# Kernel optimization log

Hardware: AMD Instinct MI355X
Metric: run time of the kernel (lower is better)

The kernel has to match this reference:

```python
import jax, jax.numpy as jnp
import numpy as np
from jax import lax

B, T, M = 32, 512, 512
D, DM, H, A = 256, 256, 256, 256  # input, memory, hidden, attention sizes
NEG = -1e30


def setup_inputs() -> dict:
    key = jax.random.key(0)
    ks = jax.random.split(key, 12)
    s = lambda k, shape, scale: jax.random.normal(k, shape, dtype=jnp.float32) * scale
    inp = {
        "inputs": s(ks[0], (B, T, D), 1.0),
        "inputs_mask": jnp.ones((B, T), dtype=bool),
        "memory": s(ks[1], (B, M, DM), 1.0),
        "memory_mask": jnp.ones((B, M), dtype=bool),
        # per-direction attention params (dir 0 = fw, 1 = bw)
        "Wm": s(ks[2], (2, DM, A), DM ** -0.5),
        "Wi": s(ks[3], (2, D, A), D ** -0.5),
        "Wh": s(ks[4], (2, H, A), H ** -0.5),
        "v": s(ks[5], (2, A), A ** -0.5),
        # per-direction GRUCell params, torch layout [3H, in] / [3H, H]
        "W_ih": s(ks[6], (2, 3 * H, D + DM), (D + DM) ** -0.5),
        "W_hh": s(ks[7], (2, 3 * H, H), H ** -0.5),
        "b_ih": s(ks[8], (2, 3 * H), 0.01),
        "b_hh": s(ks[9], (2, 3 * H), 0.01),
        # output gate: sigmoid(x @ Wg) * x on [B,T,2H]
        "Wg": s(ks[10], (2 * H, 2 * H), (2 * H) ** -0.5),
    }
    return inp


def _run_direction(xs, memory, memory_mask, Wm, Wi, Wh, v, W_ih, W_hh, b_ih, b_hh):
    # xs: [T,B,D] time-major. memory: [B,M,DM]. Returns [T,B,H].
    mem_proj = jnp.einsum("bmd,da->bma", memory, Wm)  # [B,M,A], hoisted out of loop

    def step(h, x_t):
        q = x_t @ Wi + h @ Wh                              # [B,A]
        s = jnp.einsum("bma,a->bm", jnp.tanh(mem_proj + q[:, None, :]), v)
        s = jnp.where(memory_mask, s, NEG)
        a = jax.nn.softmax(s, axis=-1)                     # [B,M]
        c = jnp.einsum("bm,bmd->bd", a, memory)            # [B,DM]
        xc = jnp.concatenate([x_t, c], axis=-1)            # [B,D+DM]
        gi = xc @ W_ih.T + b_ih
        gh = h @ W_hh.T + b_hh
        ir, iz, inn = jnp.split(gi, 3, axis=-1)
        hr, hz, hn = jnp.split(gh, 3, axis=-1)
        r = jax.nn.sigmoid(ir + hr)
        z = jax.nn.sigmoid(iz + hz)
        n = jnp.tanh(inn + r * hn)
        h_new = (1.0 - z) * n + z * h
        return h_new, h_new

    h0 = jnp.zeros((xs.shape[1], H), dtype=xs.dtype)
    _, ys = lax.scan(step, h0, xs)
    return ys


def reference(inputs, inputs_mask, memory, memory_mask, Wm, Wi, Wh, v,
              W_ih, W_hh, b_ih, b_hh, Wg):
    xs = jnp.transpose(inputs, (1, 0, 2))  # [T,B,D]
    y_fw = _run_direction(xs, memory, memory_mask, Wm[0], Wi[0], Wh[0], v[0],
                          W_ih[0], W_hh[0], b_ih[0], b_hh[0])
    y_bw = _run_direction(xs[::-1], memory, memory_mask, Wm[1], Wi[1], Wh[1], v[1],
                          W_ih[1], W_hh[1], b_ih[1], b_hh[1])[::-1]
    out = jnp.concatenate([y_fw, y_bw], axis=-1)       # [T,B,2H]
    out = jnp.transpose(out, (1, 0, 2))                # [B,T,2H]
    # Gate (dropout=0): sigmoid(W out) * out
    return jax.nn.sigmoid(out @ Wg) * out
```

## Files before the change

### kernel.cpp

```cpp
#include <hip/hip_runtime.h>
#include <stdint.h>

typedef unsigned short u16;
typedef unsigned int   u32;
typedef _Float16 half2v __attribute__((ext_vector_type(2)));

#define L2E 1.4426950408889634f
#define TWO_L2E 2.8853900817779268f

__device__ __forceinline__ float bf2f(u16 b){ return __uint_as_float(((u32)b) << 16); }
__device__ __forceinline__ float ldf(const void* p, size_t i, int flag){
  return flag ? ((const float*)p)[i] : bf2f(((const u16*)p)[i]);
}
__device__ __forceinline__ float rcpfast(float x){
#if __has_builtin(__builtin_amdgcn_rcpf)
  return __builtin_amdgcn_rcpf(x);
#else
  return 1.0f / x;
#endif
}
__device__ __forceinline__ float exp2fast(float x){
#if __has_builtin(__builtin_amdgcn_exp2f)
  return __builtin_amdgcn_exp2f(x);
#else
  return exp2f(x);
#endif
}
__device__ __forceinline__ float fdot2f(u32 a, u32 b, float c){
#if __has_builtin(__builtin_amdgcn_fdot2)
  return __builtin_amdgcn_fdot2(__builtin_bit_cast(half2v, a), __builtin_bit_cast(half2v, b), c, false);
#else
  half2v ha = __builtin_bit_cast(half2v, a), hb = __builtin_bit_cast(half2v, b);
  return c + (float)ha[0]*(float)hb[0] + (float)ha[1]*(float)hb[1];
#endif
}
__device__ __forceinline__ u32 pkh2(float lo, float hi){
  half2v h; h[0] = (_Float16)lo; h[1] = (_Float16)hi;
  return __builtin_bit_cast(u32, h);
}
__device__ __forceinline__ u16 f2h16(float f){
  _Float16 h = (_Float16)f;
  return __builtin_bit_cast(u16, h);
}
__device__ __forceinline__ float h16f(u16 h){
  return (float)__builtin_bit_cast(_Float16, h);
}

__global__ void k_sentinelf(float* __restrict__ out, int n, float val){
  int i = blockIdx.x*256 + threadIdx.x;
  if(i < n) out[i] = val;
}

__global__ void k_detect(const u16* __restrict__ p, int n, int* __restrict__ flag){
  __shared__ int cnt;
  if(threadIdx.x == 0) cnt = 0;
  __syncthreads();
  int c = 0;
  for(int i = threadIdx.x; i < n; i += 256){
    int e = (p[i] >> 7) & 0xFF;
    c += (e >= 112 && e <= 142) ? 1 : 0;
  }
  atomicAdd(&cnt, c);
  __syncthreads();
  if(threadIdx.x == 0) *flag = (cnt >= (n/10)*9) ? 0 : 1;
}
__global__ void k_convf(const void* __restrict__ src, float* __restrict__ dst, int n,
                        const int* __restrict__ flag){
  int i = blockIdx.x*256 + threadIdx.x;
  if(i < n) dst[i] = ldf(src, i, *flag);
}

__global__ void k_pack_wh2(const void* __restrict__ Wh, u32* __restrict__ out,
                           const int* __restrict__ flag){
  int i = blockIdx.x*256 + threadIdx.x;
  if(i >= 2*128*256) return;
  int d = i >> 15, k2 = (i >> 8) & 127, a = i & 255;
  float lo = ldf(Wh, ((size_t)d*256 + 2*k2    )*256 + a, *flag);
  float hi = ldf(Wh, ((size_t)d*256 + 2*k2 + 1)*256 + a, *flag);
  out[i] = pkh2(lo, hi);
}
__global__ void k_pack_wc2(const void* __restrict__ Whh, const void* __restrict__ Wih,
                           u32* __restrict__ out, const int* __restrict__ flag){
  int i = blockIdx.x*256 + threadIdx.x;
  if(i >= 2*128*2304) return;
  int d = i / (128*2304), r = i % (128*2304);
  int k2 = r / 2304, j = r % 2304;
  int k = 2*k2;
  float lo, hi;
  if(j < 768){
    lo = ldf(Whh, ((size_t)d*768 + j)*256 + k,     *flag);
    hi = ldf(Whh, ((size_t)d*768 + j)*256 + k + 1, *flag);
  } else if(j < 1536){
    lo = ldf(Wih, ((size_t)d*768 + (j-768))*512 + 256 + k,     *flag);
    hi = ldf(Wih, ((size_t)d*768 + (j-768))*512 + 256 + k + 1, *flag);
  } else {
    lo = ldf(Wih, ((size_t)d*768 + (j-1536))*512 + k,     *flag);
    hi = ldf(Wih, ((size_t)d*768 + (j-1536))*512 + k + 1, *flag);
  }
  out[i] = pkh2(lo, hi);
}
__global__ void k_pack_h2(const void* __restrict__ src, u32* __restrict__ out, int n2,
                          const int* __restrict__ flag){
  int i = blockIdx.x*256 + threadIdx.x;
  if(i >= n2) return;
  out[i] = pkh2(ldf(src, 2*(size_t)i, *flag), ldf(src, 2*(size_t)i + 1, *flag));
}
__global__ void k_pack_wiht(const void* __restrict__ Wih, float* __restrict__ out,
                            const int* __restrict__ flag){
  int i = blockIdx.x*256 + threadIdx.x;
  if(i >= 2*256*768) return;
  int d = i / 196608, r = i % 196608;
  int k = r / 768, j = r % 768;
  out[i] = ldf(Wih, ((size_t)d*768 + j)*512 + k, *flag);
}

template<int MODE>
__global__ __launch_bounds__(256)
void k_gemm_h16(const float* __restrict__ A, int lda,
                const float* __restrict__ B, int ldb,
                u16* __restrict__ C, int N, int K)
{
  __shared__ float As[64][17];
  __shared__ float Bs[16][65];
  const int m0 = blockIdx.x * 64, n0 = blockIdx.y * 64;
  const int tid = threadIdx.x;
  const int arow = tid >> 2, acol = (tid & 3) * 4;
  const int brow = tid >> 4, bcol = (tid & 15) * 4;
  const int ty = tid >> 4, tx = tid & 15;
  float acc[4][4];
  #pragma unroll
  for(int i=0;i<4;++i)
    #pragma unroll
    for(int j=0;j<4;++j) acc[i][j] = 0.f;
  for(int k0 = 0; k0 < K; k0 += 16){
    float4 a4 = *(const float4*)(A + (size_t)(m0 + arow)*lda + k0 + acol);
    As[arow][acol+0] = a4.x; As[arow][acol+1] = a4.y;
    As[arow][acol+2] = a4.z; As[arow][acol+3] = a4.w;
    float4 b4 = *(const float4*)(B + (size_t)(k0 + brow)*ldb + n0 + bcol);
    Bs[brow][bcol+0] = b4.x; Bs[brow][bcol+1] = b4.y;
    Bs[brow][bcol+2] = b4.z; Bs[brow][bcol+3] = b4.w;
    __syncthreads();
    #pragma unroll
    for(int kk = 0; kk < 16; ++kk){
      float ar[4], br[4];
      #pragma unroll
      for(int i=0;i<4;++i) ar[i] = As[ty*4+i][kk];
      #pragma unroll
      for(int j=0;j<4;++j) br[j] = Bs[kk][tx*4+j];
      #pragma unroll
      for(int i=0;i<4;++i)
        #pragma unroll
        for(int j=0;j<4;++j) acc[i][j] = fmaf(ar[i], br[j], acc[i][j]);
    }
    __syncthreads();
  }
  #pragma unroll
  for(int i=0;i<4;++i)
    #pragma unroll
    for(int j=0;j<4;++j){
      float v = acc[i][j];
      if(MODE==1){ v = exp2fast(v * TWO_L2E); v = fminf(v, 65504.f); }
      C[(size_t)(m0 + ty*4 + i)*N + n0 + tx*4 + j] = f2h16(v);
    }
}

template<int USE_GIX>
__global__ __launch_bounds__(1024)
void k_scan5(const u16* __restrict__ E16,
             const u16* __restrict__ qx16,
             const u32* __restrict__ Wh2,
             const u32* __restrict__ Wc2,
             const u32* __restrict__ xh2,
             const u16* __restrict__ gix16,
             const u32* __restrict__ memh2,
             const float* __restrict__ vf,
             const float* __restrict__ bihf,
             const float* __restrict__ bhhf,
             float* __restrict__ ys)
{
  __shared__ float h_l[256];
  __shared__ __align__(16) u32 h2[128];
  __shared__ __align__(16) u32 c2[128];
  __shared__ __align__(16) u32 x2[128];
  __shared__ __align__(16) float F[256];
  __shared__ __align__(16) float part[4096];
  __shared__ float ghgi[2304];
  __shared__ float esum_w[64];
  __shared__ float svp_sh;

  const int tid = threadIdx.x;
  const int p = blockIdx.x, d = p >> 5, b = p & 31;
  const int lane = tid & 63, wave = tid >> 6;
  const int g = lane >> 4, l = lane & 15;

  const u16* Eb   = E16  + ((size_t)d*16384 + (size_t)b*512)*256;
  const u16* qxb  = qx16 + ((size_t)d*16384 + (size_t)b*512)*256;
  const u32* Whd  = Wh2  + (size_t)d*128*256;
  const u32* Wcd  = Wc2  + (size_t)d*128*2304;
  const u32* xhb  = xh2  + (size_t)b*512*128;
  const u16* gixb = gix16 + ((size_t)d*16384 + (size_t)b*512)*768;
  const u32* mhb  = memh2 + (size_t)b*512*128;

  if(tid < 256){ h_l[tid] = 0.f; part[tid] = vf[d*256 + tid]; }
  if(tid < 128){
    h2[tid] = 0u;
    if(!USE_GIX){
      int tx0 = d ? 511 : 0;
      x2[tid] = xhb[(size_t)tx0*128 + tid];
    }
  }
  float vr[16];
  {
    const float* vp = vf + d*256 + l*16;
    *(float4*)&vr[0]  = *(const float4*)(vp);
    *(float4*)&vr[4]  = *(const float4*)(vp + 4);
    *(float4*)&vr[8]  = *(const float4*)(vp + 8);
    *(float4*)&vr[12] = *(const float4*)(vp + 12);
  }
  float bh0=0,bh1=0,bh2v=0,bi0=0,bi1=0,bi2=0;
  if(tid < 256){
    bh0  = bhhf[d*768 + tid];       bi0 = bihf[d*768 + tid];
    bh1  = bhhf[d*768 + 256 + tid]; bi1 = bihf[d*768 + 256 + tid];
    bh2v = bhhf[d*768 + 512 + tid]; bi2 = bihf[d*768 + 512 + tid];
  }
  __syncthreads();
  if(tid == 0){ float s=0.f; for(int i=0;i<256;++i) s += part[i]; svp_sh = s * L2E; }
  __syncthreads();

  auto gdot = [&](int col, const u32* s2){
    const u32* wp = Wcd + col;
    float a0=0.f, a1=0.f, a2=0.f, a3=0.f;
    #pragma unroll 4
    for(int k0=0;k0<32;++k0){
      uint4 s4 = *(const uint4*)&s2[4*k0];
      a0 = fdot2f(wp[(size_t)(4*k0    )*2304], s4.x, a0);
      a1 = fdot2f(wp[(size_t)(4*k0 + 1)*2304], s4.y, a1);
      a2 = fdot2f(wp[(size_t)(4*k0 + 2)*2304], s4.z, a2);
      a3 = fdot2f(wp[(size_t)(4*k0 + 3)*2304], s4.w, a3);
    }
    ghgi[col] = (a0+a1)+(a2+a3);
  };

  for(int step = 0; step < 512; ++step){
    const int tx = d ? (511 - step) : step;

    {
      const int a = tid & 255, kq = tid >> 8;
      const u32* wp = Whd + (size_t)(kq*32)*256 + a;
      float q0=0.f,q1=0.f,q2=0.f,q3=0.f;
      #pragma unroll
      for(int i0=0;i0<8;++i0){
        uint4 hv = *(const uint4*)&h2[kq*32 + 4*i0];
        q0 = fdot2f(wp[(size_t)(4*i0    )*256], hv.x, q0);
        q1 = fdot2f(wp[(size_t)(4*i0 + 1)*256], hv.y, q1);
        q2 = fdot2f(wp[(size_t)(4*i0 + 2)*256], hv.z, q2);
        q3 = fdot2f(wp[(size_t)(4*i0 + 3)*256], hv.w, q3);
      }
      part[kq*256 + a] = (q0+q1)+(q2+q3);
    }
    __syncthreads();
    if(tid < 256){
      float q = h16f(qxb[(size_t)tx*256 + tid])
              + part[tid] + part[256+tid] + part[512+tid] + part[768+tid];
      F[tid] = exp2fast(q * TWO_L2E);
    }
    __syncthreads();

    {
      if(tid < 768) gdot(tid, h2);
      if(!USE_GIX){
        if(tid >= 768) gdot(1536 + (tid - 768), x2);
        if(tid < 512)  gdot(1792 + tid, x2);
      }

      float Fr[16];
      {
        const float* fp = F + l*16;
        *(float4*)&Fr[0]  = *(const float4*)(fp);
        *(float4*)&Fr[4]  = *(const float4*)(fp + 4);
        *(float4*)&Fr[8]  = *(const float4*)(fp + 8);
        *(float4*)&Fr[12] = *(const float4*)(fp + 12);
      }
      float cr[16];
      #pragma unroll
      for(int i=0;i<16;++i) cr[i] = 0.f;
      float esum = 0.f;
      const float svp = svp_sh;

      #pragma unroll 2
      for(int it=0; it<8; ++it){
        const int m = wave*32 + it*4 + g;
        uint4 e0 = *(const uint4*)(Eb + (size_t)m*256 + l*16);
        uint4 e1 = *(const uint4*)(Eb + (size_t)m*256 + l*16 + 8);
        float u = 0.f;
        {
          u32 eu0=e0.x, eu1=e0.y, eu2=e0.z, eu3=e0.w;
          u32 eu4=e1.x, eu5=e1.y, eu6=e1.z, eu7=e1.w;
          #define RA_PAIR(EU, J) { \
            half2v hh = __builtin_bit_cast(half2v, EU); \
            float t0 = rcpfast(fmaf((float)hh[0], Fr[2*(J)],   1.f)); \
            float t1 = rcpfast(fmaf((float)hh[1], Fr[2*(J)+1], 1.f)); \
            u = fmaf(vr[2*(J)], t0, u); u = fmaf(vr[2*(J)+1], t1, u); }
          RA_PAIR(eu0,0) RA_PAIR(eu1,1) RA_PAIR(eu2,2) RA_PAIR(eu3,3)
          RA_PAIR(eu4,4) RA_PAIR(eu5,5) RA_PAIR(eu6,6) RA_PAIR(eu7,7)
          #undef RA_PAIR
        }
        u += __shfl_xor(u, 1, 64);
        u += __shfl_xor(u, 2, 64);
        u += __shfl_xor(u, 4, 64);
        u += __shfl_xor(u, 8, 64);
        float es = exp2fast(fmaf(u, -TWO_L2E, svp));
        esum += es;
        uint4 m0 = *(const uint4*)(mhb + (size_t)m*128 + l*8);
        uint4 m1 = *(const uint4*)(mhb + (size_t)m*128 + l*8 + 4);
        {
          u32 mu0=m0.x, mu1=m0.y, mu2=m0.z, mu3=m0.w;
          u32 mu4=m1.x, mu5=m1.y, mu6=m1.z, mu7=m1.w;
          #define RC_PAIR(MU, J) { \
            half2v hh = __builtin_bit_cast(half2v, MU); \
            cr[2*(J)]   = fmaf((float)hh[0], es, cr[2*(J)]); \
            cr[2*(J)+1] = fmaf((float)hh[1], es, cr[2*(J)+1]); }
          RC_PAIR(mu0,0) RC_PAIR(mu1,1) RC_PAIR(mu2,2) RC_PAIR(mu3,3)
          RC_PAIR(mu4,4) RC_PAIR(mu5,5) RC_PAIR(mu6,6) RC_PAIR(mu7,7)
          #undef RC_PAIR
        }
      }
      #pragma unroll
      for(int i=0;i<16;++i){
        cr[i] += __shfl_xor(cr[i], 16, 64);
        cr[i] += __shfl_xor(cr[i], 32, 64);
      }
      if(lane < 16){
        float* pp = part + wave*256 + l*16;
        *(float4*)(pp)      = make_float4(cr[0],  cr[1],  cr[2],  cr[3]);
        *(float4*)(pp + 4)  = make_float4(cr[4],  cr[5],  cr[6],  cr[7]);
        *(float4*)(pp + 8)  = make_float4(cr[8],  cr[9],  cr[10], cr[11]);
        *(float4*)(pp + 12) = make_float4(cr[12], cr[13], cr[14], cr[15]);
      }
      if(l == 0) esum_w[wave*4 + g] = esum;
    }
    __syncthreads();

    if(tid < 128){
      float rs = 0.f;
      #pragma unroll
      for(int i2=0;i2<64;++i2) rs += esum_w[i2];
      rs = rcpfast(rs);
      float lo = 0.f, hi = 0.f;
      #pragma unroll
      for(int w=0; w<16; ++w){
        lo += part[w*256 + 2*tid];
        hi += part[w*256 + 2*tid + 1];
      }
      c2[tid] = pkh2(lo*rs, hi*rs);
    }
    __syncthreads();

    if(tid < 768) gdot(768 + tid, c2);
    __syncthreads();

    if(tid < 256){
      const int j = tid;
      float hr  = ghgi[j]       + bh0;
      float hz  = ghgi[256 + j] + bh1;
      float hn  = ghgi[512 + j] + bh2v;
      float ir, iz, inn;
      if(USE_GIX){
        const u16* gxp = gixb + (size_t)tx*768;
        ir  = ghgi[768 + j]       + h16f(gxp[j])       + bi0;
        iz  = ghgi[768 + 256 + j] + h16f(gxp[256 + j]) + bi1;
        inn = ghgi[768 + 512 + j] + h16f(gxp[512 + j]) + bi2;
      } else {
        ir  = ghgi[1536 + j]       + ghgi[768 + j]       + bi0;
        iz  = ghgi[1536 + 256 + j] + ghgi[768 + 256 + j] + bi1;
        inn = ghgi[1536 + 512 + j] + ghgi[768 + 512 + j] + bi2;
      }
      float r = rcpfast(1.f + exp2fast(-(ir + hr) * L2E));
      float z = rcpfast(1.f + exp2fast(-(iz + hz) * L2E));
      float narg = inn + r*hn;
      float n = 1.f - 2.f*rcpfast(1.f + exp2fast(narg * TWO_L2E));
      float hnew = (1.f - z)*n + z*h_l[j];
      h_l[j] = hnew;
      ys[((size_t)b*512 + tx)*512 + d*256 + j] = hnew;
    }
    __syncthreads();

    if(tid < 128){
      h2[tid] = pkh2(h_l[2*tid], h_l[2*tid + 1]);
    } else if(!USE_GIX && tid < 256 && step < 511){
      int t = tid - 128;
      int txn = d ? (511 - (step+1)) : (step+1);
      x2[t] = xhb[(size_t)txn*128 + t];
    }
    __syncthreads();
  }
}

__global__ void k_gate_h(const u16* __restrict__ G, float* __restrict__ ysb, int n4){
  int i = blockIdx.x*256 + threadIdx.x;
  if(i >= n4) return;
  ushort4 g = ((const ushort4*)G)[i];
  float4 y = ((const float4*)ysb)[i];
  float4 o;
  o.x = y.x * rcpfast(1.f + exp2fast(-h16f(g.x) * L2E));
  o.y = y.y * rcpfast(1.f + exp2fast(-h16f(g.y) * L2E));
  o.z = y.z * rcpfast(1.f + exp2fast(-h16f(g.z) * L2E));
  o.w = y.w * rcpfast(1.f + exp2fast(-h16f(g.w) * L2E));
  ((float4*)ysb)[i] = o;
}

extern "C" void kernel_launch(void* const* d_in, const int* in_sizes, int n_in,
                              void* d_out, int out_size, void* d_ws, size_t ws_size,
                              hipStream_t stream)
{
  int iIn=-1, iMem=-1, iW[3]={-1,-1,-1}, nW=0, iV=-1, iWih=-1, iWhh=-1,
      iBih=-1, iBhh=-1, iWg=-1;
  for(int i = 0; i < n_in; ++i){
    switch(in_sizes[i]){
      case 4194304: if(iIn < 0) iIn = i; else if(iMem < 0) iMem = i; break;
      case 131072:  if(nW < 3) iW[nW++] = i; break;
      case 512:     iV = i; break;
      case 786432:  iWih = i; break;
      case 393216:  iWhh = i; break;
      case 1536:    if(iBih < 0) iBih = i; else if(iBhh < 0) iBhh = i; break;
      case 262144:  iWg = i; break;
      default: break;
    }
  }
  bool ok = (iIn>=0 && iMem>=0 && nW==3 && iV>=0 && iWih>=0 && iWhh>=0 &&
             iBih>=0 && iBhh>=0 && iWg>=0);
  if(!ok){
    k_sentinelf<<<(out_size + 255)/256, 256, 0, stream>>>((float*)d_out, out_size, 42.0f);
    return;
  }

  char* ws = (char*)d_ws;
  size_t off = 0;
  auto alloc = [&](size_t bytes)->void*{
    void* pp = ws + off; off += (bytes + 255) & ~(size_t)255; return pp;
  };
  float* cxf   = (float*)alloc(4194304ull*4);
  float* cmemf = (float*)alloc(4194304ull*4);
  u16*   E16   = (u16*)  alloc(2ull*16384*256*2);
  u16*   qx16  = (u16*)  alloc(2ull*16384*256*2);
  u32*   memh2 = (u32*)  alloc(32ull*512*128*4);
  u32*   Wh2   = (u32*)  alloc(2ull*128*256*4);
  u32*   Wc2   = (u32*)  alloc(2ull*128*2304*4);
  float* Wmf   = (float*)alloc(131072ull*4);
  float* Wif   = (float*)alloc(131072ull*4);
  float* Wgf   = (float*)alloc(262144ull*4);
  float* cvf   = (float*)alloc(512ull*4);
  float* bihf  = (float*)alloc(1536ull*4);
  float* bhhf  = (float*)alloc(1536ull*4);
  int*   flag  = (int*)  alloc(256);
  size_t needA = (2ull*256*768*4 + 255 + 2ull*16384*768*2 + 255);
  bool useGix = (off + needA <= ws_size);
  float* WihT  = nullptr;
  u16*   gix16 = nullptr;
  u32*   xh2   = nullptr;
  if(useGix){
    WihT  = (float*)alloc(2ull*256*768*4);
    gix16 = (u16*)  alloc(2ull*16384*768*2);
  } else {
    xh2   = (u32*)  alloc(32ull*512*128*4);
  }
  if(off > ws_size){
    k_sentinelf<<<(out_size + 255)/256, 256, 0, stream>>>((float*)d_out, out_size, 43.0f);
    return;
  }

  k_detect<<<1, 256, 0, stream>>>((const u16*)d_in[iIn], 65536, flag);

  auto conv = [&](const void* src, float* dst, int n){
    k_convf<<<(n + 255)/256, 256, 0, stream>>>(src, dst, n, flag);
  };
  conv(d_in[iIn],   cxf,   4194304);
  conv(d_in[iMem],  cmemf, 4194304);
  conv(d_in[iW[0]], Wmf,   131072);
  conv(d_in[iW[1]], Wif,   131072);
  conv(d_in[iV],    cvf,   512);
  conv(d_in[iBih],  bihf,  1536);
  conv(d_in[iBhh],  bhhf,  1536);
  conv(d_in[iWg],   Wgf,   262144);
  k_pack_wh2<<<(2*128*256 + 255)/256, 256, 0, stream>>>(d_in[iW[2]], Wh2, flag);
  k_pack_wc2<<<(2*128*2304 + 255)/256, 256, 0, stream>>>(d_in[iWhh], d_in[iWih], Wc2, flag);
  k_pack_h2<<<(2097152 + 255)/256, 256, 0, stream>>>(d_in[iMem], memh2, 2097152, flag);
  if(!useGix)
    k_pack_h2<<<(2097152 + 255)/256, 256, 0, stream>>>(d_in[iIn], xh2, 2097152, flag);
  else
    k_pack_wiht<<<(2*256*768 + 255)/256, 256, 0, stream>>>(d_in[iWih], WihT, flag);

  for(int dd = 0; dd < 2; ++dd){
    k_gemm_h16<1><<<dim3(256, 4), 256, 0, stream>>>(
        cmemf, 256, Wmf + (size_t)dd*65536, 256,
        E16 + (size_t)dd*16384*256, 256, 256);
    k_gemm_h16<0><<<dim3(256, 4), 256, 0, stream>>>(
        cxf, 256, Wif + (size_t)dd*65536, 256,
        qx16 + (size_t)dd*16384*256, 256, 256);
    if(useGix)
      k_gemm_h16<0><<<dim3(256, 12), 256, 0, stream>>>(
          cxf, 256, WihT + (size_t)dd*196608, 768,
          gix16 + (size_t)dd*16384*768, 768, 256);
  }

  if(useGix)
    k_scan5<1><<<64, 1024, 0, stream>>>(E16, qx16, Wh2, Wc2, nullptr, gix16, memh2,
                                        cvf, bihf, bhhf, (float*)d_out);
  else
    k_scan5<0><<<64, 1024, 0, stream>>>(E16, qx16, Wh2, Wc2, xh2, nullptr, memh2,
                                        cvf, bihf, bhhf, (float*)d_out);

  u16* G16 = (u16*)cxf;
  k_gemm_h16<0><<<dim3(256, 8), 256, 0, stream>>>(
      (const float*)d_out, 512, Wgf, 512, G16, 512, 512);
  k_gate_h<<<(8388608/4 + 255)/256, 256, 0, stream>>>(G16, (float*)d_out, 8388608/4);
}
```

Baseline: 10.19 ms.

## Stage memory in LDS and overlap hidden GEMV with Wh projection in scan

Adds a new scan kernel for the precomputed-gix path. It copies half of the per-batch fp16 memory tile into 128KB of dynamic LDS, and waves 0-7 read the context operand from there instead of global memory. The Wh query projection now runs on 256 threads concurrently with the h-side GRU GEMV on the other 768 threads, which removes one barrier per step. The packed h2 state is written straight from the update step via a shuffle, saving another barrier. The cost is very high LDS use (about 157KB), more work per thread in the q projection, and uneven load across waves.

After: 10.81 ms. +6.1%, slower.

```diff
diff --git a/kernel.cpp b/kernel.cpp
--- a/kernel.cpp
+++ b/kernel.cpp
@@ -164,19 +164,223 @@
     }
 }
 
-template<int USE_GIX>
+#define SCAN6_LDS 156944
 __global__ __launch_bounds__(1024)
-void k_scan5(const u16* __restrict__ E16,
+void k_scan6(const u16* __restrict__ E16,
              const u16* __restrict__ qx16,
              const u32* __restrict__ Wh2,
              const u32* __restrict__ Wc2,
-             const u32* __restrict__ xh2,
              const u16* __restrict__ gix16,
              const u32* __restrict__ memh2,
              const float* __restrict__ vf,
              const float* __restrict__ bihf,
              const float* __restrict__ bhhf,
              float* __restrict__ ys)
+{
+  extern __shared__ char smem[];
+  u32*   meml   = (u32*)(smem);
+  float* part   = (float*)(smem + 131072);
+  float* ghgi   = (float*)(smem + 147456);
+  float* F      = (float*)(smem + 153600);
+  float* h_l    = (float*)(smem + 154624);
+  u32*   h2     = (u32*)(smem + 155648);
+  u32*   c2     = (u32*)(smem + 156160);
+  float* esum_w = (float*)(smem + 156672);
+  float* svp_p  = (float*)(smem + 156928);
+
+  const int tid = threadIdx.x;
+  const int p = blockIdx.x, d = p >> 5, b = p & 31;
+  const int lane = tid & 63, wave = tid >> 6;
+  const int g = lane >> 4, l = lane & 15;
+
+  const u16* Eb   = E16   + ((size_t)d*16384 + (size_t)b*512)*256;
+  const u16* qxb  = qx16  + ((size_t)d*16384 + (size_t)b*512)*256;
+  const u32* Whd  = Wh2   + (size_t)d*128*256;
+  const u32* Wcd  = Wc2   + (size_t)d*128*2304;
+  const u16* gixb = gix16 + ((size_t)d*16384 + (size_t)b*512)*768;
+  const u32* mhb  = memh2 + (size_t)b*512*128;
+
+  {
+    const uint4* mg = (const uint4*)mhb;
+    uint4* md = (uint4*)meml;
+    for(int i = tid; i < 8192; i += 1024) md[i] = mg[i];
+  }
+  if(tid < 256) h_l[tid] = 0.f;
+  if(tid < 128) h2[tid] = 0u;
+  float vr[16];
+  {
+    const float* vp = vf + d*256 + l*16;
+    *(float4*)&vr[0]  = *(const float4*)(vp);
+    *(float4*)&vr[4]  = *(const float4*)(vp + 4);
+    *(float4*)&vr[8]  = *(const float4*)(vp + 8);
+    *(float4*)&vr[12] = *(const float4*)(vp + 12);
+  }
+  if(tid == 0){
+    float s = 0.f;
+    for(int i=0;i<256;++i) s += vf[d*256 + i];
+    svp_p[0] = s * L2E;
+  }
+  float bh0=0,bh1=0,bh2v=0,bi0=0,bi1=0,bi2=0;
+  if(tid < 256){
+    bh0  = bhhf[d*768 + tid];       bi0 = bihf[d*768 + tid];
+    bh1  = bhhf[d*768 + 256 + tid]; bi1 = bihf[d*768 + 256 + tid];
+    bh2v = bhhf[d*768 + 512 + tid]; bi2 = bihf[d*768 + 512 + tid];
+  }
+  __syncthreads();
+
+  auto gdot = [&](int col, const u32* s2){
+    const u32* wp = Wcd + col;
+    float a0=0.f, a1=0.f, a2=0.f, a3=0.f;
+    #pragma unroll 4
+    for(int k0=0;k0<32;++k0){
+      uint4 s4 = *(const uint4*)&s2[4*k0];
+      a0 = fdot2f(wp[(size_t)(4*k0    )*2304], s4.x, a0);
+      a1 = fdot2f(wp[(size_t)(4*k0 + 1)*2304], s4.y, a1);
+      a2 = fdot2f(wp[(size_t)(4*k0 + 2)*2304], s4.z, a2);
+      a3 = fdot2f(wp[(size_t)(4*k0 + 3)*2304], s4.w, a3);
+    }
+    ghgi[col] = (a0+a1)+(a2+a3);
+  };
+
+  for(int step = 0; step < 512; ++step){
+    const int tx = d ? (511 - step) : step;
+
+    if(tid < 256){
+      const u32* wp = Whd + tid;
+      float q0=0.f,q1=0.f,q2=0.f,q3=0.f;
+      #pragma unroll 4
+      for(int k0=0;k0<32;++k0){
+        uint4 hv = *(const uint4*)&h2[4*k0];
+        q0 = fdot2f(wp[(size_t)(4*k0    )*256], hv.x, q0);
+        q1 = fdot2f(wp[(size_t)(4*k0 + 1)*256], hv.y, q1);
+        q2 = fdot2f(wp[(size_t)(4*k0 + 2)*256], hv.z, q2);
+        q3 = fdot2f(wp[(size_t)(4*k0 + 3)*256], hv.w, q3);
+      }
+      float q = h16f(qxb[(size_t)tx*256 + tid]) + (q0+q1)+(q2+q3);
+      F[tid] = exp2fast(q * TWO_L2E);
+    } else {
+      gdot(tid - 256, h2);
+    }
+    __syncthreads();
+
+    {
+      float Fr[16];
+      {
+        const float* fp = F + l*16;
+        *(float4*)&Fr[0]  = *(const float4*)(fp);
+        *(float4*)&Fr[4]  = *(const float4*)(fp + 4);
+        *(float4*)&Fr[8]  = *(const float4*)(fp + 8);
+        *(float4*)&Fr[12] = *(const float4*)(fp + 12);
+      }
+      float cr[16];
+      #pragma unroll
+      for(int i=0;i<16;++i) cr[i] = 0.f;
+      float esum = 0.f;
+      const float svp = svp_p[0];
+
+      #pragma unroll 2
+      for(int it=0; it<8; ++it){
+        const int m = wave*32 + it*4 + g;
+        uint4 e0 = *(const uint4*)(Eb + (size_t)m*256 + l*16);
+        uint4 e1 = *(const uint4*)(Eb + (size_t)m*256 + l*16 + 8);
+        float u = 0.f;
+        {
+          #define RA_PAIR(EU, J) { \
+            half2v hh = __builtin_bit_cast(half2v, EU); \
+            float t0 = rcpfast(fmaf((float)hh[0], Fr[2*(J)],   1.f)); \
+            float t1 = rcpfast(fmaf((float)hh[1], Fr[2*(J)+1], 1.f)); \
+            u = fmaf(vr[2*(J)], t0, u); u = fmaf(vr[2*(J)+1], t1, u); }
+          RA_PAIR(e0.x,0) RA_PAIR(e0.y,1) RA_PAIR(e0.z,2) RA_PAIR(e0.w,3)
+          RA_PAIR(e1.x,4) RA_PAIR(e1.y,5) RA_PAIR(e1.z,6) RA_PAIR(e1.w,7)
+          #undef RA_PAIR
+        }
+        u += __shfl_xor(u, 1, 64);
+        u += __shfl_xor(u, 2, 64);
+        u += __shfl_xor(u, 4, 64);
+        u += __shfl_xor(u, 8, 64);
+        float es = exp2fast(fmaf(u, -TWO_L2E, svp));
+        esum += es;
+        uint4 m0, m1;
+        if(wave < 8){
+          m0 = *(const uint4*)&meml[(size_t)m*128 + l*8];
+          m1 = *(const uint4*)&meml[(size_t)m*128 + l*8 + 4];
+        } else {
+          m0 = *(const uint4*)(mhb + (size_t)m*128 + l*8);
+          m1 = *(const uint4*)(mhb + (size_t)m*128 + l*8 + 4);
+        }
+        {
+          #define RC_PAIR(MU, J) { \
+            half2v hh = __builtin_bit_cast(half2v, MU); \
+            cr[2*(J)]   = fmaf((float)hh[0], es, cr[2*(J)]); \
+            cr[2*(J)+1] = fmaf((float)hh[1], es, cr[2*(J)+1]); }
+          RC_PAIR(m0.x,0) RC_PAIR(m0.y,1) RC_PAIR(m0.z,2) RC_PAIR(m0.w,3)
+          RC_PAIR(m1.x,4) RC_PAIR(m1.y,5) RC_PAIR(m1.z,6) RC_PAIR(m1.w,7)
+          #undef RC_PAIR
+        }
+      }
+      #pragma unroll
+      for(int i=0;i<16;++i){
+        cr[i] += __shfl_xor(cr[i], 16, 64);
+        cr[i] += __shfl_xor(cr[i], 32, 64);
+      }
+      if(lane < 16){
+        float* pp = part + wave*256 + l*16;
+        *(float4*)(pp)      = make_float4(cr[0],  cr[1],  cr[2],  cr[3]);
+        *(float4*)(pp + 4)  = make_float4(cr[4],  cr[5],  cr[6],  cr[7]);
+        *(float4*)(pp + 8)  = make_float4(cr[8],  cr[9],  cr[10], cr[11]);
+        *(float4*)(pp + 12) = make_float4(cr[12], cr[13], cr[14], cr[15]);
+      }
+      if(l == 0) esum_w[wave*4 + g] = esum;
+    }
+    __syncthreads();
+
+    if(tid < 128){
+      float rs = 0.f;
+      #pragma unroll
+      for(int i2=0;i2<64;++i2) rs += esum_w[i2];
+      rs = rcpfast(rs);
+      float lo = 0.f, hi = 0.f;
+      #pragma unroll
+      for(int w=0; w<16; ++w){
+        lo += part[w*256 + 2*tid];
+        hi += part[w*256 + 2*tid + 1];
+      }
+      c2[tid] = pkh2(lo*rs, hi*rs);
+    }
+    __syncthreads();
+
+    if(tid < 768) gdot(768 + tid, c2);
+    __syncthreads();
+
+    if(tid < 256){
+      const int j = tid;
+      const u16* gxp = gixb + (size_t)tx*768;
+      float hr  = ghgi[j]       + bh0;
+      float hz  = ghgi[256 + j] + bh1;
+      float hn  = ghgi[512 + j] + bh2v;
+      float ir  = ghgi[768 + j]       + h16f(gxp[j])       + bi0;
+      float iz  = ghgi[768 + 256 + j] + h16f(gxp[256 + j]) + bi1;
+      float inn = ghgi[768 + 512 + j] + h16f(gxp[512 + j]) + bi2;
+      float r = rcpfast(1.f + exp2fast(-(ir + hr) * L2E));
+      float z = rcpfast(1.f + exp2fast(-(iz + hz) * L2E));
+      float narg = inn + r*hn;
+      float n = 1.f - 2.f*rcpfast(1.f + exp2fast(narg * TWO_L2E));
+      float hnew = (1.f - z)*n + z*h_l[j];
+      h_l[j] = hnew;
+      ys[((size_t)b*512 + tx)*512 + d*256 + j] = hnew;
+      float hpart = __shfl_xor(hnew, 1, 64);
+      if((j & 1) == 0) h2[j >> 1] = pkh2(hnew, hpart);
+    }
+    __syncthreads();
+  }
+}
+
+__global__ __launch_bounds__(1024)
+void k_scan5b(const u16* __restrict__ E16, const u16* __restrict__ qx16,
+              const u32* __restrict__ Wh2, const u32* __restrict__ Wc2,
+              const u32* __restrict__ xh2, const u32* __restrict__ memh2,
+              const float* __restrict__ vf, const float* __restrict__ bihf,
+              const float* __restrict__ bhhf, float* __restrict__ ys)
 {
   __shared__ float h_l[256];
   __shared__ __align__(16) u32 h2[128];
@@ -193,21 +397,18 @@
   const int lane = tid & 63, wave = tid >> 6;
   const int g = lane >> 4, l = lane & 15;
 
-  const u16* Eb   = E16  + ((size_t)d*16384 + (size_t)b*512)*256;
-  const u16* qxb  = qx16 + ((size_t)d*16384 + (size_t)b*512)*256;
-  const u32* Whd  = Wh2  + (size_t)d*128*256;
-  const u32* Wcd  = Wc2  + (size_t)d*128*2304;
-  const u32* xhb  = xh2  + (size_t)b*512*128;
-  const u16* gixb = gix16 + ((size_t)d*16384 + (size_t)b*512)*768;
-  const u32* mhb  = memh2 + (size_t)b*512*128;
+  const u16* Eb  = E16  + ((size_t)d*16384 + (size_t)b*512)*256;
+  const u16* qxb = qx16 + ((size_t)d*16384 + (size_t)b*512)*256;
+  const u32* Whd = Wh2  + (size_t)d*128*256;
+  const u32* Wcd = Wc2  + (size_t)d*128*2304;
+  const u32* xhb = xh2  + (size_t)b*512*128;
+  const u32* mhb = memh2 + (size_t)b*512*128;
 
   if(tid < 256){ h_l[tid] = 0.f; part[tid] = vf[d*256 + tid]; }
   if(tid < 128){
     h2[tid] = 0u;
-    if(!USE_GIX){
-      int tx0 = d ? 511 : 0;
-      x2[tid] = xhb[(size_t)tx0*128 + tid];
-    }
+    int tx0 = d ? 511 : 0;
+    x2[tid] = xhb[(size_t)tx0*128 + tid];
   }
   float vr[16];
   {
@@ -243,7 +444,6 @@
 
   for(int step = 0; step < 512; ++step){
     const int tx = d ? (511 - step) : step;
-
     {
       const int a = tid & 255, kq = tid >> 8;
       const u32* wp = Whd + (size_t)(kq*32)*256 + a;
@@ -265,13 +465,10 @@
       F[tid] = exp2fast(q * TWO_L2E);
     }
     __syncthreads();
-
     {
       if(tid < 768) gdot(tid, h2);
-      if(!USE_GIX){
-        if(tid >= 768) gdot(1536 + (tid - 768), x2);
-        if(tid < 512)  gdot(1792 + tid, x2);
-      }
+      if(tid >= 768) gdot(1536 + (tid - 768), x2);
+      if(tid < 512)  gdot(1792 + tid, x2);
 
       float Fr[16];
       {
@@ -286,7 +483,6 @@
       for(int i=0;i<16;++i) cr[i] = 0.f;
       float esum = 0.f;
       const float svp = svp_sh;
-
       #pragma unroll 2
       for(int it=0; it<8; ++it){
         const int m = wave*32 + it*4 + g;
@@ -294,15 +490,13 @@
         uint4 e1 = *(const uint4*)(Eb + (size_t)m*256 + l*16 + 8);
         float u = 0.f;
         {
-          u32 eu0=e0.x, eu1=e0.y, eu2=e0.z, eu3=e0.w;
-          u32 eu4=e1.x, eu5=e1.y, eu6=e1.z, eu7=e1.w;
           #define RA_PAIR(EU, J) { \
             half2v hh = __builtin_bit_cast(half2v, EU); \
             float t0 = rcpfast(fmaf((float)hh[0], Fr[2*(J)],   1.f)); \
             float t1 = rcpfast(fmaf((float)hh[1], Fr[2*(J)+1], 1.f)); \
             u = fmaf(vr[2*(J)], t0, u); u = fmaf(vr[2*(J)+1], t1, u); }
-          RA_PAIR(eu0,0) RA_PAIR(eu1,1) RA_PAIR(eu2,2) RA_PAIR(eu3,3)
-          RA_PAIR(eu4,4) RA_PAIR(eu5,5) RA_PAIR(eu6,6) RA_PAIR(eu7,7)
+          RA_PAIR(e0.x,0) RA_PAIR(e0.y,1) RA_PAIR(e0.z,2) RA_PAIR(e0.w,3)
+          RA_PAIR(e1.x,4) RA_PAIR(e1.y,5) RA_PAIR(e1.z,6) RA_PAIR(e1.w,7)
           #undef RA_PAIR
         }
         u += __shfl_xor(u, 1, 64);
@@ -314,14 +508,12 @@
         uint4 m0 = *(const uint4*)(mhb + (size_t)m*128 + l*8);
         uint4 m1 = *(const uint4*)(mhb + (size_t)m*128 + l*8 + 4);
         {
-          u32 mu0=m0.x, mu1=m0.y, mu2=m0.z, mu3=m0.w;
-          u32 mu4=m1.x, mu5=m1.y, mu6=m1.z, mu7=m1.w;
           #define RC_PAIR(MU, J) { \
             half2v hh = __builtin_bit_cast(half2v, MU); \
             cr[2*(J)]   = fmaf((float)hh[0], es, cr[2*(J)]); \
             cr[2*(J)+1] = fmaf((float)hh[1], es, cr[2*(J)+1]); }
-          RC_PAIR(mu0,0) RC_PAIR(mu1,1) RC_PAIR(mu2,2) RC_PAIR(mu3,3)
-          RC_PAIR(mu4,4) RC_PAIR(mu5,5) RC_PAIR(mu6,6) RC_PAIR(mu7,7)
+          RC_PAIR(m0.x,0) RC_PAIR(m0.y,1) RC_PAIR(m0.z,2) RC_PAIR(m0.w,3)
+          RC_PAIR(m1.x,4) RC_PAIR(m1.y,5) RC_PAIR(m1.z,6) RC_PAIR(m1.w,7)
           #undef RC_PAIR
         }
       }
@@ -340,7 +532,6 @@
       if(l == 0) esum_w[wave*4 + g] = esum;
     }
     __syncthreads();
-
     if(tid < 128){
       float rs = 0.f;
       #pragma unroll
@@ -355,26 +546,16 @@
       c2[tid] = pkh2(lo*rs, hi*rs);
     }
     __syncthreads();
-
     if(tid < 768) gdot(768 + tid, c2);
     __syncthreads();
-
     if(tid < 256){
       const int j = tid;
       float hr  = ghgi[j]       + bh0;
       float hz  = ghgi[256 + j] + bh1;
       float hn  = ghgi[512 + j] + bh2v;
-      float ir, iz, inn;
-      if(USE_GIX){
-        const u16* gxp = gixb + (size_t)tx*768;
-        ir  = ghgi[768 + j]       + h16f(gxp[j])       + bi0;
-        iz  = ghgi[768 + 256 + j] + h16f(gxp[256 + j]) + bi1;
-        inn = ghgi[768 + 512 + j] + h16f(gxp[512 + j]) + bi2;
-      } else {
-        ir  = ghgi[1536 + j]       + ghgi[768 + j]       + bi0;
-        iz  = ghgi[1536 + 256 + j] + ghgi[768 + 256 + j] + bi1;
-        inn = ghgi[1536 + 512 + j] + ghgi[768 + 512 + j] + bi2;
-      }
+      float ir  = ghgi[1536 + j]       + ghgi[768 + j]       + bi0;
+      float iz  = ghgi[1536 + 256 + j] + ghgi[768 + 256 + j] + bi1;
+      float inn = ghgi[1536 + 512 + j] + ghgi[768 + 512 + j] + bi2;
       float r = rcpfast(1.f + exp2fast(-(ir + hr) * L2E));
       float z = rcpfast(1.f + exp2fast(-(iz + hz) * L2E));
       float narg = inn + r*hn;
@@ -384,10 +565,9 @@
       ys[((size_t)b*512 + tx)*512 + d*256 + j] = hnew;
     }
     __syncthreads();
-
     if(tid < 128){
       h2[tid] = pkh2(h_l[2*tid], h_l[2*tid + 1]);
-    } else if(!USE_GIX && tid < 256 && step < 511){
+    } else if(tid < 256 && step < 511){
       int t = tid - 128;
       int txn = d ? (511 - (step+1)) : (step+1);
       x2[t] = xhb[(size_t)txn*128 + t];
@@ -503,12 +683,15 @@
           gix16 + (size_t)dd*16384*768, 768, 256);
   }
 
-  if(useGix)
-    k_scan5<1><<<64, 1024, 0, stream>>>(E16, qx16, Wh2, Wc2, nullptr, gix16, memh2,
-                                        cvf, bihf, bhhf, (float*)d_out);
-  else
-    k_scan5<0><<<64, 1024, 0, stream>>>(E16, qx16, Wh2, Wc2, xh2, nullptr, memh2,
-                                        cvf, bihf, bhhf, (float*)d_out);
+  if(useGix){
+    (void)hipFuncSetAttribute((const void*)k_scan6,
+                              hipFuncAttributeMaxDynamicSharedMemorySize, SCAN6_LDS);
+    k_scan6<<<64, 1024, SCAN6_LDS, stream>>>(E16, qx16, Wh2, Wc2, gix16, memh2,
+                                             cvf, bihf, bhhf, (float*)d_out);
+  } else {
+    k_scan5b<<<64, 1024, 0, stream>>>(E16, qx16, Wh2, Wc2, xh2, memh2,
+                                      cvf, bihf, bhhf, (float*)d_out);
+  }
 
   u16* G16 = (u16*)cxf;
   k_gemm_h16<0><<<dim3(256, 8), 256, 0, stream>>>(
```
